# Kernel tuning notes

Measured on AMD Instinct MI355X. Metric: run time of the kernel, lower is better.

The kernel has to match this reference:

```python
import jax, jax.numpy as jnp
import numpy as np

# Dims: node hidden = (VO vectors, SO scalars); messages = (VEC_IN vectors, S_M scalars)
VO, SO, VEC_IN, S_M = 16, 100, 17, 132
B, N, K = 4, 2048, 30


def _split(x, nv):
    # flat [..., 3*nv + ns] -> vectors [..., 3, nv], scalars [..., ns]
    v = x[..., :3 * nv].reshape(x.shape[:-1] + (3, nv))
    return v, x[..., 3 * nv:]


def _merge(v, s):
    return jnp.concatenate([v.reshape(v.shape[:-2] + (3 * v.shape[-1],)), s], -1)


def _norm_no_nan(x, axis=-1, keepdims=False, eps=1e-8, sqrt=True):
    out = jnp.maximum(jnp.sum(x * x, axis=axis, keepdims=keepdims), eps)
    return jnp.sqrt(out) if sqrt else out


def _vs_concat(x1, x2, nv1, nv2):
    v1, s1 = _split(x1, nv1)
    v2, s2 = _split(x2, nv2)
    return _merge(jnp.concatenate([v1, v2], -1), jnp.concatenate([s1, s2], -1))


def _gvp(x, nv_in, wh, ws, bs, wv, act=True):
    # Geometric Vector Perceptron: nls=relu on scalars, nlv=sigmoid gate on vector norms.
    v, s = _split(x, nv_in)
    vh = jnp.einsum('...ci,ih->...ch', v, wh)        # c = 3 spatial dims
    vn = _norm_no_nan(vh, axis=-2)                    # [..., h]
    s_out = jnp.concatenate([s, vn], -1) @ ws + bs
    if act:
        s_out = jax.nn.relu(s_out)
    v_out = jnp.einsum('...ch,ho->...co', vh, wv)
    if act:
        v_out = v_out * jax.nn.sigmoid(_norm_no_nan(v_out, axis=-2, keepdims=True))
    return _merge(v_out, s_out)


def _gvp_layernorm(x, nv, gamma, beta, eps=1e-3):
    # scalars: standard LayerNorm (keras default eps=1e-3); vectors: divide by RMS of channel norms
    v, s = _split(x, nv)
    vn2 = _norm_no_nan(v, axis=-2, keepdims=True, sqrt=False)      # [..., 1, nv]
    v = v / jnp.sqrt(jnp.mean(vn2, axis=-1, keepdims=True))
    mu = jnp.mean(s, -1, keepdims=True)
    var = jnp.mean((s - mu) ** 2, -1, keepdims=True)
    s = (s - mu) * jax.lax.rsqrt(var + eps) * gamma + beta
    return _merge(v, s)


def _dense(key, fan_in, fan_out):
    return jax.random.normal(key, (fan_in, fan_out), jnp.float32) / np.sqrt(fan_in)


def setup_inputs() -> dict:
    key = jax.random.key(0)
    ks = jax.random.split(key, 20)
    d = {
        'h_V': jax.random.normal(ks[0], (B, N, 3 * VO + SO), jnp.float32),
        'h_M': jax.random.normal(ks[1], (B, N, K, 3 * VEC_IN + S_M), jnp.float32),
        'mask_V': jnp.ones((B, N), jnp.int32),
        'mask_attend': jnp.ones((B, N, K), jnp.int32),
    }
    # W_EV: GVP(33->16, 232->100), GVP(16->16, 100->100), GVP(16->16, 100->100, no act)
    d['wev1_wh'] = _dense(ks[2], 33, 33)
    d['wev1_ws'] = _dense(ks[3], 232 + 33, 100)
    d['wev1_bs'] = jnp.zeros((100,), jnp.float32)
    d['wev1_wv'] = _dense(ks[4], 33, 16)
    d['wev2_wh'] = _dense(ks[5], 16, 16)
    d['wev2_ws'] = _dense(ks[6], 116, 100)
    d['wev2_bs'] = jnp.zeros((100,), jnp.float32)
    d['wev2_wv'] = _dense(ks[7], 16, 16)
    d['wev3_wh'] = _dense(ks[8], 16, 16)
    d['wev3_ws'] = _dense(ks[9], 116, 100)
    d['wev3_bs'] = jnp.zeros((100,), jnp.float32)
    d['wev3_wv'] = _dense(ks[10], 16, 16)
    # W_dh: GVP(16->32, 100->400), GVP(32->16, 400->100, no act)
    d['wdh1_wh'] = _dense(ks[11], 16, 32)
    d['wdh1_ws'] = _dense(ks[12], 100 + 32, 400)
    d['wdh1_bs'] = jnp.zeros((400,), jnp.float32)
    d['wdh1_wv'] = _dense(ks[13], 32, 32)
    d['wdh2_wh'] = _dense(ks[14], 32, 32)
    d['wdh2_ws'] = _dense(ks[15], 400 + 32, 100)
    d['wdh2_bs'] = jnp.zeros((100,), jnp.float32)
    d['wdh2_wv'] = _dense(ks[16], 32, 16)
    d['ln1_g'] = jnp.ones((100,), jnp.float32)
    d['ln1_b'] = jnp.zeros((100,), jnp.float32)
    d['ln2_g'] = jnp.ones((100,), jnp.float32)
    d['ln2_b'] = jnp.zeros((100,), jnp.float32)
    return d


def reference(h_V, h_M, mask_V, mask_attend,
              wev1_wh, wev1_ws, wev1_bs, wev1_wv,
              wev2_wh, wev2_ws, wev2_bs, wev2_wv,
              wev3_wh, wev3_ws, wev3_bs, wev3_wv,
              wdh1_wh, wdh1_ws, wdh1_bs, wdh1_wv,
              wdh2_wh, wdh2_ws, wdh2_bs, wdh2_wv,
              ln1_g, ln1_b, ln2_g, ln2_b):
    # tile node features along neighbor axis, concat with messages
    h_V_exp = jnp.broadcast_to(h_V[..., None, :], h_M.shape[:-1] + (h_V.shape[-1],))
    h_EV = _vs_concat(h_V_exp, h_M, VO, VEC_IN)                   # [B,N,K, 3*33 + 232]
    m = _gvp(h_EV, VO + VEC_IN, wev1_wh, wev1_ws, wev1_bs, wev1_wv)
    m = _gvp(m, VO, wev2_wh, wev2_ws, wev2_bs, wev2_wv)
    m = _gvp(m, VO, wev3_wh, wev3_ws, wev3_bs, wev3_wv, act=False)
    m = mask_attend[..., None].astype(jnp.float32) * m
    dh = jnp.mean(m, axis=-2)                                     # reduce over neighbors
    hv = _gvp_layernorm(h_V + dh, VO, ln1_g, ln1_b)               # dropout inactive (train=False)
    dh = _gvp(hv, VO, wdh1_wh, wdh1_ws, wdh1_bs, wdh1_wv)
    dh = _gvp(dh, 2 * VO, wdh2_wh, wdh2_ws, wdh2_bs, wdh2_wv, act=False)
    hv = _gvp_layernorm(hv + dh, VO, ln2_g, ln2_b)
    return mask_V[..., None].astype(jnp.float32) * hv
```

## Files before the change

### kernel.cpp

```cpp
#include <hip/hip_runtime.h>
#include <math.h>

#define NT 256

typedef __attribute__((ext_vector_type(8))) short short8;
typedef __attribute__((ext_vector_type(4))) float float4v;

struct P28 {
    const float *h_V, *h_M;
    const int *mask_V, *mask_attend;
    const float *w1h,*w1s,*b1,*w1v;
    const float *w2h,*w2s,*b2,*w2v;
    const float *w3h,*w3s,*b3,*w3v;
    const float *d1h,*d1s,*db1,*d1v;
    const float *d2h,*d2s,*db2,*d2v;
    const float *g1,*be1,*g2,*be2;
    float *out, *dh;
    short *wt1, *wt2, *wt3;
};

__device__ inline short f2bf(float f) {
    union { float f; unsigned u; } v; v.f = f;
    unsigned r = (v.u + 0x7FFFu + ((v.u >> 16) & 1u)) >> 16;
    return (short)r;
}

__device__ void gemm(const float* A0, int split, const float* A1, int KA,
                     const float* uni, int uniK,
                     const float* Bg, int ldB, int N,
                     const float* bias, bool relu,
                     float* outL, int MP, float* Bbuf, int bbf, int tid)
{
    const bool vec = ((N & 3) == 0) && ((ldB & 3) == 0);
    const int Npad = vec ? N : ((N + 3) & ~3);
    const int EQ = MP >> 2;
    const int npairs = EQ * (Npad >> 2);
    const int Ktot = uniK + KA;
    int KC = bbf / Npad;
    if (KC > Ktot) KC = Ktot;

    const bool active = tid < npairs;
    const int e0 = (active ? (tid % EQ) : 0) * 4;
    const int j0 = (active ? (tid / EQ) : 0) * 4;

    float c00=0.f,c01=0.f,c02=0.f,c03=0.f;
    float c10=0.f,c11=0.f,c12=0.f,c13=0.f;
    float c20=0.f,c21=0.f,c22=0.f,c23=0.f;
    float c30=0.f,c31=0.f,c32=0.f,c33=0.f;
    float su0=0.f,su1=0.f,su2=0.f,su3=0.f;

    float4 r0, r1, r2, r3;
    r0.x=r0.y=r0.z=r0.w=0.f; r1=r0; r2=r0; r3=r0;

    if (vec) {
        int kc0 = (KC < Ktot) ? KC : Ktot;
        int nf4 = (kc0 * N) >> 2;
        int f4 = tid;
        if (f4 < nf4) { int f = f4*4; int k = f / N; r0 = *(const float4*)(Bg + (size_t)k*ldB + (f - k*N)); }
        f4 = tid + NT;
        if (f4 < nf4) { int f = f4*4; int k = f / N; r1 = *(const float4*)(Bg + (size_t)k*ldB + (f - k*N)); }
        f4 = tid + 2*NT;
        if (f4 < nf4) { int f = f4*4; int k = f / N; r2 = *(const float4*)(Bg + (size_t)k*ldB + (f - k*N)); }
        f4 = tid + 3*NT;
        if (f4 < nf4) { int f = f4*4; int k = f / N; r3 = *(const float4*)(Bg + (size_t)k*ldB + (f - k*N)); }
    }

    for (int k0 = 0; k0 < Ktot; k0 += KC) {
        int kc = Ktot - k0; if (kc > KC) kc = KC;
        __syncthreads();
        if (vec) {
            int nf4 = (kc * N) >> 2;
            float4* Bb4 = (float4*)Bbuf;
            if (tid        < nf4) Bb4[tid]        = r0;
            if (tid +   NT < nf4) Bb4[tid +   NT] = r1;
            if (tid + 2*NT < nf4) Bb4[tid + 2*NT] = r2;
            if (tid + 3*NT < nf4) Bb4[tid + 3*NT] = r3;
            int k0n = k0 + KC;
            if (k0n < Ktot) {
                int kcn = Ktot - k0n; if (kcn > KC) kcn = KC;
                int nf4n = (kcn * N) >> 2;
                const float* Bn = Bg + (size_t)k0n * ldB;
                int f4 = tid;
                if (f4 < nf4n) { int f = f4*4; int k = f / N; r0 = *(const float4*)(Bn + (size_t)k*ldB + (f - k*N)); }
                f4 = tid + NT;
                if (f4 < nf4n) { int f = f4*4; int k = f / N; r1 = *(const float4*)(Bn + (size_t)k*ldB + (f - k*N)); }
                f4 = tid + 2*NT;
                if (f4 < nf4n) { int f = f4*4; int k = f / N; r2 = *(const float4*)(Bn + (size_t)k*ldB + (f - k*N)); }
                f4 = tid + 3*NT;
                if (f4 < nf4n) { int f = f4*4; int k = f / N; r3 = *(const float4*)(Bn + (size_t)k*ldB + (f - k*N)); }
            }
        } else {
            for (int idx = tid; idx < kc * Npad; idx += NT) {
                int k = idx / Npad, j = idx - k * Npad;
                Bbuf[idx] = (j < N) ? Bg[(size_t)(k0 + k) * ldB + j] : 0.f;
            }
        }
        __syncthreads();
        if (active) {
            for (int k = 0; k < kc; ++k) {
                int kg = k0 + k;
                float4 b4 = *(const float4*)(Bbuf + k * Npad + j0);
                if (kg < uniK) {
                    float u = uni[kg];
                    su0 = fmaf(u, b4.x, su0); su1 = fmaf(u, b4.y, su1);
                    su2 = fmaf(u, b4.z, su2); su3 = fmaf(u, b4.w, su3);
                } else {
                    int ka = kg - uniK;
                    const float* arow = (ka < split) ? (A0 + (size_t)ka * MP + e0)
                                                     : (A1 + (size_t)(ka - split) * MP + e0);
                    float4 a4 = *(const float4*)arow;
                    c00 = fmaf(a4.x, b4.x, c00); c01 = fmaf(a4.y, b4.x, c01);
                    c02 = fmaf(a4.z, b4.x, c02); c03 = fmaf(a4.w, b4.x, c03);
                    c10 = fmaf(a4.x, b4.y, c10); c11 = fmaf(a4.y, b4.y, c11);
                    c12 = fmaf(a4.z, b4.y, c12); c13 = fmaf(a4.w, b4.y, c13);
                    c20 = fmaf(a4.x, b4.z, c20); c21 = fmaf(a4.y, b4.z, c21);
                    c22 = fmaf(a4.z, b4.z, c22); c23 = fmaf(a4.w, b4.z, c23);
                    c30 = fmaf(a4.x, b4.w, c30); c31 = fmaf(a4.y, b4.w, c31);
                    c32 = fmaf(a4.z, b4.w, c32); c33 = fmaf(a4.w, b4.w, c33);
                }
            }
        }
    }
    __syncthreads();
    if (active) {
        float4 o;
        if (j0 + 0 < N) {
            float s = su0 + (bias ? bias[j0 + 0] : 0.f);
            o.x = c00 + s; o.y = c01 + s; o.z = c02 + s; o.w = c03 + s;
            if (relu) { o.x = fmaxf(o.x,0.f); o.y = fmaxf(o.y,0.f); o.z = fmaxf(o.z,0.f); o.w = fmaxf(o.w,0.f); }
            *(float4*)(outL + (size_t)(j0 + 0) * MP + e0) = o;
        }
        if (j0 + 1 < N) {
            float s = su1 + (bias ? bias[j0 + 1] : 0.f);
            o.x = c10 + s; o.y = c11 + s; o.z = c12 + s; o.w = c13 + s;
            if (relu) { o.x = fmaxf(o.x,0.f); o.y = fmaxf(o.y,0.f); o.z = fmaxf(o.z,0.f); o.w = fmaxf(o.w,0.f); }
            *(float4*)(outL + (size_t)(j0 + 1) * MP + e0) = o;
        }
        if (j0 + 2 < N) {
            float s = su2 + (bias ? bias[j0 + 2] : 0.f);
            o.x = c20 + s; o.y = c21 + s; o.z = c22 + s; o.w = c23 + s;
            if (relu) { o.x = fmaxf(o.x,0.f); o.y = fmaxf(o.y,0.f); o.z = fmaxf(o.z,0.f); o.w = fmaxf(o.w,0.f); }
            *(float4*)(outL + (size_t)(j0 + 2) * MP + e0) = o;
        }
        if (j0 + 3 < N) {
            float s = su3 + (bias ? bias[j0 + 3] : 0.f);
            o.x = c30 + s; o.y = c31 + s; o.z = c32 + s; o.w = c33 + s;
            if (relu) { o.x = fmaxf(o.x,0.f); o.y = fmaxf(o.y,0.f); o.z = fmaxf(o.z,0.f); o.w = fmaxf(o.w,0.f); }
            *(float4*)(outL + (size_t)(j0 + 3) * MP + e0) = o;
        }
    }
}

__device__ void vn_dev(const float* vh, int nch, int MP, int cs,
                       float* out, int ostr, int tid)
{
    for (int idx = tid; idx < nch * cs; idx += NT) {
        int h = idx / cs, e = idx - h * cs;
        float a = vh[h * MP + e], b = vh[h * MP + cs + e], c = vh[h * MP + 2 * cs + e];
        out[h * ostr + e] = sqrtf(fmaxf(a * a + b * b + c * c, 1e-8f));
    }
}

__device__ void gate_dev(float* vb, int nch, int MP, int cs, int tid)
{
    for (int idx = tid; idx < nch * cs; idx += NT) {
        int o = idx / cs, e = idx - o * cs;
        float* b = vb + o * MP + e;
        float a = b[0], b1 = b[cs], c = b[2 * cs];
        float n = sqrtf(fmaxf(a * a + b1 * b1 + c * c, 1e-8f));
        float g = 1.f / (1.f + expf(-n));
        b[0] = a * g; b[cs] = b1 * g; b[2 * cs] = c * g;
    }
}

__device__ void mfma_gemm(const short* Alds, int Astr, const short* Bg, int Kpad,
                          int ktiles, const float* bias,
                          short* outA, int outAstr,
                          float* Sred, const float* maskf, int tid)
{
    const int w = tid >> 6, lane = tid & 63;
    const int q = lane >> 4, l16 = lane & 15;
    for (int t = w; t < 14; t += 4) {
        int mt = t & 1, nt = t >> 1;
        const short* ap = Alds + (mt * 16 + l16) * Astr + q * 8;
        const short* bp = Bg + (size_t)(nt * 16 + l16) * Kpad + q * 8;
        float4v acc = {0.f, 0.f, 0.f, 0.f};
        for (int kt = 0; kt < ktiles; ++kt) {
            short8 a = *(const short8*)(ap + kt * 32);
            short8 b = *(const short8*)(bp + kt * 32);
            acc = __builtin_amdgcn_mfma_f32_16x16x32_bf16(a, b, acc, 0, 0, 0);
        }
        int j = nt * 16 + l16;
        if (j < 100) {
            float bj = bias ? bias[j] : 0.f;
            int ebase = mt * 16 + q * 4;
            if (outA) {
                for (int r = 0; r < 4; ++r) {
                    float v = fmaxf(acc[r] + bj, 0.f);
                    outA[(ebase + r) * outAstr + j] = f2bf(v);
                }
            } else {
                float part = 0.f;
                for (int r = 0; r < 4; ++r) part += maskf[ebase + r] * (acc[r] + bj);
                atomicAdd(&Sred[j], part);
            }
        }
    }
}

__global__ __launch_bounds__(NT) void prep_w(P28 p)
{
    int id = blockIdx.x * NT + threadIdx.x;
    int stride = gridDim.x * NT;
    for (int i = id; i < 112 * 192; i += stride) {
        int n = i / 192, k = i - n * 192;
        float v = 0.f;
        if (n < 100) {
            int row = -1;
            if (k < 132) row = 100 + k;
            else if (k < 165) row = 232 + (k - 132);
            if (row >= 0) v = p.w1s[(size_t)row * 100 + n];
        }
        p.wt1[i] = f2bf(v);
    }
    for (int i = id; i < 112 * 128; i += stride) {
        int n = i / 128, k = i - n * 128;
        p.wt2[i] = f2bf((n < 100 && k < 116) ? p.w2s[(size_t)k * 100 + n] : 0.f);
    }
    for (int i = id; i < 112 * 128; i += stride) {
        int n = i / 128, k = i - n * 128;
        p.wt3[i] = f2bf((n < 100 && k < 116) ? p.w3s[(size_t)k * 100 + n] : 0.f);
    }
}

__global__ __launch_bounds__(NT) void edge_kernel(P28 p)
{
    __shared__ __align__(16) short A1s[32 * 200];
    __shared__ __align__(16) float vhb[33 * 96];
    __shared__ __align__(16) short A2s[32 * 136];
    __shared__ __align__(16) float Bbuf[1200];
    __shared__ float Sred[100];
    __shared__ float ubias[100];
    __shared__ float maskf[32];

    short* A3s = A1s;

    const int node = blockIdx.x, tid = threadIdx.x;
    const float* hV = p.h_V + (size_t)node * 148;

    for (int i = tid; i < 32; i += NT)
        maskf[i] = (i < 30) ? (float)p.mask_attend[(size_t)node * 30 + i] : 0.f;
    for (int i = tid; i < 100; i += NT) Sred[i] = 0.f;
    for (int idx = tid; idx < 32 * 132; idx += NT) {
        int e = idx / 132, k = idx - e * 132;
        float v = (e < 30) ? p.h_M[((size_t)node * 30 + e) * 183 + 51 + k] : 0.f;
        A1s[e * 200 + k] = f2bf(v);
    }
    for (int idx = tid; idx < 32 * 27; idx += NT) {
        int kk = idx >> 5, e = idx & 31;
        A1s[e * 200 + 165 + kk] = 0;
    }
    for (int idx = tid; idx < 32 * 12; idx += NT) {
        int kk = idx >> 5, e = idx & 31;
        A2s[e * 136 + 116 + kk] = 0;
    }
    for (int idx = tid; idx < 33 * 96; idx += NT) {
        int i = idx / 96, r = idx - i * 96, c = r >> 5, e = r & 31;
        float v = 0.f;
        if (i < 16) v = hV[c * 16 + i];
        else if (e < 30) v = p.h_M[((size_t)node * 30 + e) * 183 + c * 17 + (i - 16)];
        vhb[idx] = v;
    }
    for (int j = tid; j < 100; j += NT) {
        float s = p.b1[j];
        for (int i = 0; i < 100; ++i)
            s = fmaf(hV[48 + i], p.w1s[(size_t)i * 100 + j], s);
        ubias[j] = s;
    }
    __syncthreads();

    gemm(vhb, 33, nullptr, 33, nullptr, 0, p.w1h, 33, 33, nullptr, false, vhb, 96, Bbuf, 1200, tid);
    __syncthreads();
    for (int idx = tid; idx < 33 * 32; idx += NT) {
        int h = idx >> 5, e = idx & 31;
        float a = vhb[h * 96 + e], b = vhb[h * 96 + 32 + e], c = vhb[h * 96 + 64 + e];
        A1s[e * 200 + 132 + h] = f2bf(sqrtf(fmaxf(a * a + b * b + c * c, 1e-8f)));
    }
    __syncthreads();
    gemm(vhb, 33, nullptr, 33, nullptr, 0, p.w1v, 16, 16, nullptr, false, vhb, 96, Bbuf, 1200, tid);
    __syncthreads();
    gate_dev(vhb, 16, 96, 32, tid);
    mfma_gemm(A1s, 200, p.wt1, 192, 6, ubias, A2s, 136, nullptr, nullptr, tid);
    __syncthreads();

    gemm(vhb, 16, nullptr, 16, nullptr, 0, p.w2h, 16, 16, nullptr, false, vhb + 16 * 96, 96, Bbuf, 1200, tid);
    __syncthreads();
    for (int idx = tid; idx < 16 * 32; idx += NT) {
        int h = idx >> 5, e = idx & 31;
        float a = vhb[(16 + h) * 96 + e], b = vhb[(16 + h) * 96 + 32 + e], c = vhb[(16 + h) * 96 + 64 + e];
        A2s[e * 136 + 100 + h] = f2bf(sqrtf(fmaxf(a * a + b * b + c * c, 1e-8f)));
    }
    for (int idx = tid; idx < 32 * 12; idx += NT) {
        int kk = idx >> 5, e = idx & 31;
        A3s[e * 136 + 116 + kk] = 0;
    }
    __syncthreads();
    gemm(vhb + 16 * 96, 16, nullptr, 16, nullptr, 0, p.w2v, 16, 16, nullptr, false, vhb, 96, Bbuf, 1200, tid);
    __syncthreads();
    gate_dev(vhb, 16, 96, 32, tid);
    mfma_gemm(A2s, 136, p.wt2, 128, 4, p.b2, A3s, 136, nullptr, nullptr, tid);
    __syncthreads();

    gemm(vhb, 16, nullptr, 16, nullptr, 0, p.w3h, 16, 16, nullptr, false, vhb + 16 * 96, 96, Bbuf, 1200, tid);
    __syncthreads();
    for (int idx = tid; idx < 16 * 32; idx += NT) {
        int h = idx >> 5, e = idx & 31;
        float a = vhb[(16 + h) * 96 + e], b = vhb[(16 + h) * 96 + 32 + e], c = vhb[(16 + h) * 96 + 64 + e];
        A3s[e * 136 + 100 + h] = f2bf(sqrtf(fmaxf(a * a + b * b + c * c, 1e-8f)));
    }
    __syncthreads();
    gemm(vhb + 16 * 96, 16, nullptr, 16, nullptr, 0, p.w3v, 16, 16, nullptr, false, vhb, 96, Bbuf, 1200, tid);
    __syncthreads();
    mfma_gemm(A3s, 136, p.wt3, 128, 4, p.b3, nullptr, 0, Sred, maskf, tid);
    __syncthreads();

    float* dhn = p.dh + (size_t)node * 148;
    for (int f = tid; f < 148; f += NT) {
        float s;
        if (f < 48) {
            int c = f >> 4, o = f & 15;
            const float* src = vhb + o * 96 + c * 32;
            float acc = 0.f;
            int e = f % 30;
            for (int t = 0; t < 30; ++t) { acc += maskf[e] * src[e]; if (++e == 30) e = 0; }
            s = acc;
        } else {
            s = Sred[f - 48];
        }
        dhn[f] = s * (1.f / 30.f);
    }
}

__global__ __launch_bounds__(NT) void node_kernel(P28 p)
{
    __shared__ __align__(16) float Bbuf[3200];
    __shared__ __align__(16) float S1n[132 * 16];
    __shared__ __align__(16) float A2n[400 * 16];
    __shared__ __align__(16) float s2n[100 * 16];
    __shared__ __align__(16) float hvv[16 * 48];
    __shared__ __align__(16) float vhA[32 * 48];
    __shared__ __align__(16) float vhB[32 * 48];
    __shared__ float mu[16], isd[16], vrm[16], mkv[16];

    const int nb = blockIdx.x * 16;
    const int tid = threadIdx.x;

    for (int idx = tid; idx < 1600; idx += NT) {
        int n = idx & 15, j = idx >> 4;
        size_t g = (size_t)(nb + n) * 148 + 48 + j;
        S1n[idx] = p.h_V[g] + p.dh[g];
    }
    for (int idx = tid; idx < 768; idx += NT) {
        int i = idx / 48, r = idx - i * 48, c = r >> 4, n = r & 15;
        size_t g = (size_t)(nb + n) * 148 + c * 16 + i;
        hvv[idx] = p.h_V[g] + p.dh[g];
    }
    for (int i = tid; i < 16; i += NT) mkv[i] = (float)p.mask_V[nb + i];
    __syncthreads();

    if (tid < 16) {
        int n = tid;
        float sm = 0.f;
        for (int j = 0; j < 100; ++j) sm += S1n[j * 16 + n];
        float m = sm * 0.01f, var = 0.f;
        for (int j = 0; j < 100; ++j) { float d = S1n[j * 16 + n] - m; var += d * d; }
        mu[n] = m; isd[n] = rsqrtf(var * 0.01f + 1e-3f);
        float vm = 0.f;
        for (int i = 0; i < 16; ++i) {
            float a = hvv[i * 48 + n], b = hvv[i * 48 + 16 + n], c = hvv[i * 48 + 32 + n];
            vm += fmaxf(a * a + b * b + c * c, 1e-8f);
        }
        vrm[n] = rsqrtf(vm * (1.f / 16.f));
    }
    __syncthreads();
    for (int idx = tid; idx < 1600; idx += NT) {
        int n = idx & 15, j = idx >> 4;
        S1n[idx] = (S1n[idx] - mu[n]) * isd[n] * p.g1[j] + p.be1[j];
    }
    for (int idx = tid; idx < 768; idx += NT) hvv[idx] *= vrm[idx & 15];
    __syncthreads();

    gemm(hvv, 16, nullptr, 16, nullptr, 0, p.d1h, 32, 32, nullptr, false, vhA, 48, Bbuf, 3200, tid);
    __syncthreads();
    vn_dev(vhA, 32, 48, 16, S1n + 100 * 16, 16, tid);
    __syncthreads();
    gemm(S1n, 132, nullptr, 132, nullptr, 0, p.d1s,       400, 200, p.db1,       true, A2n,            16, Bbuf, 3200, tid);
    gemm(S1n, 132, nullptr, 132, nullptr, 0, p.d1s + 200, 400, 200, p.db1 + 200, true, A2n + 200 * 16, 16, Bbuf, 3200, tid);
    gemm(vhA, 32, nullptr, 32, nullptr, 0, p.d1v, 32, 32, nullptr, false, vhB, 48, Bbuf, 3200, tid);
    __syncthreads();
    gate_dev(vhB, 32, 48, 16, tid);
    __syncthreads();

    gemm(vhB, 32, nullptr, 32, nullptr, 0, p.d2h, 32, 32, nullptr, false, vhA, 48, Bbuf, 3200, tid);
    __syncthreads();
    vn_dev(vhA, 32, 48, 16, S1n + 100 * 16, 16, tid);
    __syncthreads();
    gemm(A2n, 400, S1n + 100 * 16, 432, nullptr, 0, p.d2s, 100, 100, p.db2, false, s2n, 16, Bbuf, 3200, tid);
    gemm(vhA, 32, nullptr, 32, nullptr, 0, p.d2v, 16, 16, nullptr, false, vhB, 48, Bbuf, 3200, tid);
    __syncthreads();

    for (int idx = tid; idx < 1600; idx += NT) s2n[idx] += S1n[idx];
    for (int idx = tid; idx < 768; idx += NT) vhB[idx] += hvv[idx];
    __syncthreads();

    if (tid < 16) {
        int n = tid;
        float sm = 0.f;
        for (int j = 0; j < 100; ++j) sm += s2n[j * 16 + n];
        float m = sm * 0.01f, var = 0.f;
        for (int j = 0; j < 100; ++j) { float d = s2n[j * 16 + n] - m; var += d * d; }
        mu[n] = m; isd[n] = rsqrtf(var * 0.01f + 1e-3f);
        float vm = 0.f;
        for (int i = 0; i < 16; ++i) {
            float a = vhB[i * 48 + n], b = vhB[i * 48 + 16 + n], c = vhB[i * 48 + 32 + n];
            vm += fmaxf(a * a + b * b + c * c, 1e-8f);
        }
        vrm[n] = rsqrtf(vm * (1.f / 16.f));
    }
    __syncthreads();
    for (int idx = tid; idx < 1600; idx += NT) {
        int n = idx & 15, j = idx >> 4;
        s2n[idx] = (s2n[idx] - mu[n]) * isd[n] * p.g2[j] + p.be2[j];
    }
    for (int idx = tid; idx < 768; idx += NT) vhB[idx] *= vrm[idx & 15];
    __syncthreads();

    for (int idx = tid; idx < 16 * 148; idx += NT) {
        int n = idx / 148, f = idx - n * 148;
        float v;
        if (f < 48) { int c = f >> 4, o = f & 15; v = vhB[o * 48 + c * 16 + n]; }
        else        { v = s2n[(f - 48) * 16 + n]; }
        p.out[(size_t)(nb + n) * 148 + f] = mkv[n] * v;
    }
}

extern "C" void kernel_launch(void* const* d_in, const int* in_sizes, int n_in,
                              void* d_out, int out_size, void* d_ws, size_t ws_size,
                              hipStream_t stream)
{
    P28 p;
    p.h_V = (const float*)d_in[0];
    p.h_M = (const float*)d_in[1];
    p.mask_V = (const int*)d_in[2];
    p.mask_attend = (const int*)d_in[3];
    const float** w = (const float**)&p.w1h;
    for (int i = 0; i < 24; ++i) w[i] = (const float*)d_in[4 + i];
    p.out = (float*)d_out;
    p.dh  = (float*)d_out;
    p.wt1 = (short*)d_ws;
    p.wt2 = p.wt1 + 112 * 192;
    p.wt3 = p.wt2 + 112 * 128;

    prep_w<<<dim3(64), dim3(NT), 0, stream>>>(p);
    edge_kernel<<<dim3(8192), dim3(NT), 0, stream>>>(p);
    node_kernel<<<dim3(512),  dim3(NT), 0, stream>>>(p);
}
```

Before: 782.0 us.

## Preload all vector-channel weights into shared memory and simplify per-layer vector GEMMs

All small vector-channel weight matrices (w1h padded to 36 columns, w1v, w2h, w2v, w3h, w3v) are loaded once into a shared buffer at kernel start. The generic per-call staged GEMM is replaced by a leaner register-tiled gemm_c that reads weights straight from shared memory and holds an internal barrier before writing in place. Several explicit __syncthreads before vector GEMMs are dropped because gemm_c syncs internally. This removes repeated global weight staging and barriers per GEMM, at the cost of more shared memory per block.

```diff
diff --git a/kernel.cpp b/kernel.cpp
--- a/kernel.cpp
+++ b/kernel.cpp
@@ -151,6 +151,57 @@
     }
 }
 
+__device__ void gemm_c(const float* A, int Ktot,
+                       const float* Bl, int ldB, int N, int Nst,
+                       float* outL, int MP, int tid)
+{
+    const int EQ = MP >> 2;
+    const int npairs = EQ * (N >> 2);
+    const bool active = tid < npairs;
+    const int e0 = (active ? (tid % EQ) : 0) * 4;
+    const int j0 = (active ? (tid / EQ) : 0) * 4;
+
+    float c00=0.f,c01=0.f,c02=0.f,c03=0.f;
+    float c10=0.f,c11=0.f,c12=0.f,c13=0.f;
+    float c20=0.f,c21=0.f,c22=0.f,c23=0.f;
+    float c30=0.f,c31=0.f,c32=0.f,c33=0.f;
+
+    if (active) {
+        for (int k = 0; k < Ktot; ++k) {
+            float4 a4 = *(const float4*)(A + (size_t)k * MP + e0);
+            float4 b4 = *(const float4*)(Bl + (size_t)k * ldB + j0);
+            c00 = fmaf(a4.x, b4.x, c00); c01 = fmaf(a4.y, b4.x, c01);
+            c02 = fmaf(a4.z, b4.x, c02); c03 = fmaf(a4.w, b4.x, c03);
+            c10 = fmaf(a4.x, b4.y, c10); c11 = fmaf(a4.y, b4.y, c11);
+            c12 = fmaf(a4.z, b4.y, c12); c13 = fmaf(a4.w, b4.y, c13);
+            c20 = fmaf(a4.x, b4.z, c20); c21 = fmaf(a4.y, b4.z, c21);
+            c22 = fmaf(a4.z, b4.z, c22); c23 = fmaf(a4.w, b4.z, c23);
+            c30 = fmaf(a4.x, b4.w, c30); c31 = fmaf(a4.y, b4.w, c31);
+            c32 = fmaf(a4.z, b4.w, c32); c33 = fmaf(a4.w, b4.w, c33);
+        }
+    }
+    __syncthreads();
+    if (active) {
+        float4 o;
+        if (j0 + 0 < Nst) {
+            o.x = c00; o.y = c01; o.z = c02; o.w = c03;
+            *(float4*)(outL + (size_t)(j0 + 0) * MP + e0) = o;
+        }
+        if (j0 + 1 < Nst) {
+            o.x = c10; o.y = c11; o.z = c12; o.w = c13;
+            *(float4*)(outL + (size_t)(j0 + 1) * MP + e0) = o;
+        }
+        if (j0 + 2 < Nst) {
+            o.x = c20; o.y = c21; o.z = c22; o.w = c23;
+            *(float4*)(outL + (size_t)(j0 + 2) * MP + e0) = o;
+        }
+        if (j0 + 3 < Nst) {
+            o.x = c30; o.y = c31; o.z = c32; o.w = c33;
+            *(float4*)(outL + (size_t)(j0 + 3) * MP + e0) = o;
+        }
+    }
+}
+
 __device__ void vn_dev(const float* vh, int nch, int MP, int cs,
                        float* out, int ostr, int tid)
 {
@@ -238,7 +289,7 @@
     __shared__ __align__(16) short A1s[32 * 200];
     __shared__ __align__(16) float vhb[33 * 96];
     __shared__ __align__(16) short A2s[32 * 136];
-    __shared__ __align__(16) float Bbuf[1200];
+    __shared__ __align__(16) float wc[2740];
     __shared__ float Sred[100];
     __shared__ float ubias[100];
     __shared__ float maskf[32];
@@ -271,6 +322,15 @@
         else if (e < 30) v = p.h_M[((size_t)node * 30 + e) * 183 + c * 17 + (i - 16)];
         vhb[idx] = v;
     }
+    for (int i = tid; i < 33 * 36; i += NT) {
+        int k = i / 36, j = i - k * 36;
+        wc[i] = (j < 33) ? p.w1h[(size_t)k * 33 + j] : 0.f;
+    }
+    for (int i = tid; i < 528; i += NT) wc[1188 + i] = p.w1v[i];
+    for (int i = tid; i < 256; i += NT) wc[1716 + i] = p.w2h[i];
+    for (int i = tid; i < 256; i += NT) wc[1972 + i] = p.w2v[i];
+    for (int i = tid; i < 256; i += NT) wc[2228 + i] = p.w3h[i];
+    for (int i = tid; i < 256; i += NT) wc[2484 + i] = p.w3v[i];
     for (int j = tid; j < 100; j += NT) {
         float s = p.b1[j];
         for (int i = 0; i < 100; ++i)
@@ -279,21 +339,20 @@
     }
     __syncthreads();
 
-    gemm(vhb, 33, nullptr, 33, nullptr, 0, p.w1h, 33, 33, nullptr, false, vhb, 96, Bbuf, 1200, tid);
+    gemm_c(vhb, 33, wc, 36, 36, 33, vhb, 96, tid);
     __syncthreads();
     for (int idx = tid; idx < 33 * 32; idx += NT) {
         int h = idx >> 5, e = idx & 31;
         float a = vhb[h * 96 + e], b = vhb[h * 96 + 32 + e], c = vhb[h * 96 + 64 + e];
         A1s[e * 200 + 132 + h] = f2bf(sqrtf(fmaxf(a * a + b * b + c * c, 1e-8f)));
     }
-    __syncthreads();
-    gemm(vhb, 33, nullptr, 33, nullptr, 0, p.w1v, 16, 16, nullptr, false, vhb, 96, Bbuf, 1200, tid);
+    gemm_c(vhb, 33, wc + 1188, 16, 16, 16, vhb, 96, tid);
     __syncthreads();
     gate_dev(vhb, 16, 96, 32, tid);
     mfma_gemm(A1s, 200, p.wt1, 192, 6, ubias, A2s, 136, nullptr, nullptr, tid);
     __syncthreads();
 
-    gemm(vhb, 16, nullptr, 16, nullptr, 0, p.w2h, 16, 16, nullptr, false, vhb + 16 * 96, 96, Bbuf, 1200, tid);
+    gemm_c(vhb, 16, wc + 1716, 16, 16, 16, vhb + 16 * 96, 96, tid);
     __syncthreads();
     for (int idx = tid; idx < 16 * 32; idx += NT) {
         int h = idx >> 5, e = idx & 31;
@@ -304,22 +363,20 @@
         int kk = idx >> 5, e = idx & 31;
         A3s[e * 136 + 116 + kk] = 0;
     }
-    __syncthreads();
-    gemm(vhb + 16 * 96, 16, nullptr, 16, nullptr, 0, p.w2v, 16, 16, nullptr, false, vhb, 96, Bbuf, 1200, tid);
+    gemm_c(vhb + 16 * 96, 16, wc + 1972, 16, 16, 16, vhb, 96, tid);
     __syncthreads();
     gate_dev(vhb, 16, 96, 32, tid);
     mfma_gemm(A2s, 136, p.wt2, 128, 4, p.b2, A3s, 136, nullptr, nullptr, tid);
     __syncthreads();
 
-    gemm(vhb, 16, nullptr, 16, nullptr, 0, p.w3h, 16, 16, nullptr, false, vhb + 16 * 96, 96, Bbuf, 1200, tid);
+    gemm_c(vhb, 16, wc + 2228, 16, 16, 16, vhb + 16 * 96, 96, tid);
     __syncthreads();
     for (int idx = tid; idx < 16 * 32; idx += NT) {
         int h = idx >> 5, e = idx & 31;
         float a = vhb[(16 + h) * 96 + e], b = vhb[(16 + h) * 96 + 32 + e], c = vhb[(16 + h) * 96 + 64 + e];
         A3s[e * 136 + 100 + h] = f2bf(sqrtf(fmaxf(a * a + b * b + c * c, 1e-8f)));
     }
-    __syncthreads();
-    gemm(vhb + 16 * 96, 16, nullptr, 16, nullptr, 0, p.w3v, 16, 16, nullptr, false, vhb, 96, Bbuf, 1200, tid);
+    gemm_c(vhb + 16 * 96, 16, wc + 2484, 16, 16, 16, vhb, 96, tid);
     __syncthreads();
     mfma_gemm(A3s, 136, p.wt3, 128, 4, p.b3, nullptr, 0, Sred, maskf, tid);
     __syncthreads();
```

After: 770.3 us. About the same (-1.5%).
